# Kernel tuning notes

Hardware: AMD Instinct MI355X
Metric: run time of the kernel (lower is better)

Reference implementation:

```python
import jax
import jax.numpy as jnp
import numpy as np
from jax import lax

B, L, A, C = 32, 128, 64, 128  # batch, length, n_agents, channels (in == out)
KT = 3                          # temporal kernel size, padding (KT-1)//2 keeps length


def setup_inputs() -> dict:
    key = jax.random.key(0)
    k1, k2, k3 = jax.random.split(key, 3)
    x = jax.random.normal(k1, (B, L, A, C), dtype=jnp.float32)
    # Conv2d weight [out_ch, in_ch, kt, 1] and bias, kaiming-ish scale
    W = jax.random.normal(k2, (C, C, KT, 1), dtype=jnp.float32) * (1.0 / np.sqrt(C * KT))
    b = jax.random.normal(k3, (C,), dtype=jnp.float32) * 0.01
    return {"x": x, "W": W, "b": b}


def reference(x, W, b):
    # x: [B, L, A, C] -> [B, C, L, A] (torch NCHW layout with H=time, W=agents)
    length, n_agents = x.shape[1], x.shape[2]
    xc = jnp.transpose(x, (0, 3, 1, 2))
    res = xc  # residual is identity (input_dim == output_dim, t_stride == 1)
    pad_t = (KT - 1) // 2
    y = lax.conv_general_dilated(
        xc, W,
        window_strides=(1, 1),
        padding=[(pad_t, pad_t), (0, 0)],
        dimension_numbers=("NCHW", "OIHW", "NCHW"),
    ) + b[None, :, None, None]  # [B, C, L, A]
    # Dense graph g[t,a,t',a'] = 1 iff t==t' or a==a'.  einsum('ncv,vw->ncw', x, g)
    # is exactly: sum over same time (all agents) + sum over same agent (all times) - self.
    agent_sum = jnp.sum(y, axis=3, keepdims=True)  # [B, C, L, 1]
    time_sum = jnp.sum(y, axis=2, keepdims=True)   # [B, C, 1, A]
    scale = (length + n_agents - 2) ** 0.5
    g = (agent_sum + time_sum - y) / scale
    out = jax.nn.relu(g + res)
    return jnp.transpose(out, (0, 2, 3, 1))  # [B, L, A, C]
```

## Files before the change

### kernel.cpp

```cpp
#include <hip/hip_runtime.h>
#include <stdint.h>


typedef __attribute__((ext_vector_type(8))) short bf16x8;
typedef __attribute__((ext_vector_type(4))) float f32x4;

__device__ __forceinline__ uint32_t f2bf(float f) {
    union { float f; uint32_t u; } v; v.f = f;
    return (v.u + 0x7FFFu + ((v.u >> 16) & 1u)) >> 16;
}
__device__ __forceinline__ float bf2f(uint32_t h) {
    union { uint32_t u; float f; } v; v.u = h << 16; return v.f;
}
__device__ __forceinline__ uint32_t pk2(float lo, float hi) {
    return f2bf(lo) | (f2bf(hi) << 16);
}
__device__ __forceinline__ void gll16(const void* g, void* l) {
    __builtin_amdgcn_global_load_lds((const __attribute__((address_space(1))) void*)g,
                                     (__attribute__((address_space(3))) void*)l, 16, 0, 0);
}

__global__ __launch_bounds__(256) void prep_kernel(
    const float* __restrict__ x, uint16_t* __restrict__ x16, uint16_t* __restrict__ xa16,
    const float* __restrict__ W, uint16_t* __restrict__ wp)
{
    const int tid = threadIdx.x;
    const int bid = blockIdx.x;
    if (bid >= 4160) {
        int o = (bid - 4160) * 256 + tid;
        int i = o & 7, lane = (o >> 3) & 63, nt = (o >> 9) & 7, ks = (o >> 12) & 3, d = o >> 14;
        int ci = ks * 32 + (lane >> 4) * 8 + i;
        int co = nt * 16 + (lane & 15);
        wp[o] = (uint16_t)f2bf(W[(co * 128 + ci) * 3 + d]);
        return;
    }
    const int b = bid / 130, tp = bid - b * 130;
    uint16_t* xo = x16 + (size_t)bid * 8192;
    if (tp == 0 || tp == 129) {
        const uint4 z = make_uint4(0, 0, 0, 0);
        #pragma unroll
        for (int k = 0; k < 4; ++k) *(uint4*)(xo + tid * 32 + k * 8) = z;
        if (tid < 16) *(uint4*)(xa16 + (size_t)bid * 128 + tid * 8) = z;
        return;
    }
    const int t = tp - 1;
    const int ci4 = (tid & 31) * 4, ag = tid >> 5;
    const float* xr = x + (size_t)(b * 128 + t) * 8192;
    float4 part = make_float4(0.f, 0.f, 0.f, 0.f);
    #pragma unroll
    for (int r = 0; r < 8; ++r) {
        const int a = ag * 8 + r;
        const float4 v = *(const float4*)(xr + a * 128 + ci4);
        part.x += v.x; part.y += v.y; part.z += v.z; part.w += v.w;
        uint2 p; p.x = pk2(v.x, v.y); p.y = pk2(v.z, v.w);
        *(uint2*)(xo + a * 128 + ci4) = p;
    }
    __shared__ float red[8][128];
    *(float4*)&red[ag][ci4] = part;
    __syncthreads();
    if (tid < 128) {
        float s = 0.f;
        #pragma unroll
        for (int i = 0; i < 8; ++i) s += red[i][tid];
        xa16[(size_t)bid * 128 + tid] = (uint16_t)f2bf(s);
    }
}

__global__ __launch_bounds__(256) void xt_kernel(
    const uint16_t* __restrict__ x16, float* __restrict__ xt)
{
    const int tid = threadIdx.x, bid = blockIdx.x;
    const int a = bid & 63, b = bid >> 6;
    const int ci8 = (tid & 15) * 8, tg = tid >> 4;
    const uint16_t* base = x16 + ((size_t)(b * 130 + 1 + tg) * 64 + a) * 128 + ci8;
    float s[8];
    #pragma unroll
    for (int j = 0; j < 8; ++j) s[j] = 0.f;
    #pragma unroll
    for (int r = 0; r < 8; ++r) {
        const uint4 v = *(const uint4*)(base + (size_t)r * 16 * 8192);
        s[0] += bf2f(v.x & 0xFFFFu); s[1] += bf2f(v.x >> 16);
        s[2] += bf2f(v.y & 0xFFFFu); s[3] += bf2f(v.y >> 16);
        s[4] += bf2f(v.z & 0xFFFFu); s[5] += bf2f(v.z >> 16);
        s[6] += bf2f(v.w & 0xFFFFu); s[7] += bf2f(v.w >> 16);
    }
    __shared__ float red[16][128];
    *(float4*)&red[tg][ci8]     = make_float4(s[0], s[1], s[2], s[3]);
    *(float4*)&red[tg][ci8 + 4] = make_float4(s[4], s[5], s[6], s[7]);
    __syncthreads();
    if (tid < 128) {
        float v = 0.f;
        #pragma unroll
        for (int i = 0; i < 16; ++i) v += red[i][tid];
        xt[(size_t)bid * 128 + tid] = v;
    }
}

__global__ __launch_bounds__(256, 2) void sums_kernel(
    const uint16_t* __restrict__ xa16, const float* __restrict__ xt,
    const uint16_t* __restrict__ x16, const uint16_t* __restrict__ wp,
    const float* __restrict__ bias, float* __restrict__ asum, float* __restrict__ tsum)
{
    __shared__ __align__(16) uint16_t slab[130 * 128];
    const int tid = threadIdx.x;
    const int lane = tid & 63, wid = tid >> 6;
    const int wm = wid >> 1, wn = wid & 1;
    const int lr = lane & 15, lg = lane >> 4;
    f32x4 acc[4][4];
    #pragma unroll
    for (int mi = 0; mi < 4; ++mi)
        #pragma unroll
        for (int ni = 0; ni < 4; ++ni) acc[mi][ni] = (f32x4)0.f;

    if (blockIdx.x < 32) {
        const int b = blockIdx.x;
        #pragma unroll
        for (int it = 0; it < 9; ++it) {
            const int gg = it * 256 + tid;
            if (gg < 2080) {
                const int row = gg >> 4, sp = gg & 15;
                const int sl = sp ^ (row & 7);
                *(uint4*)(slab + gg * 8) =
                    *(const uint4*)(xa16 + (size_t)(b * 130 + row) * 128 + sl * 8);
            }
        }
        __syncthreads();
        #pragma unroll
        for (int g = 0; g < 4; ++g)
            #pragma unroll
            for (int d = 0; d < 3; ++d) {
                bf16x8 bq[4], af[4];
                #pragma unroll
                for (int ni = 0; ni < 4; ++ni)
                    bq[ni] = *(const bf16x8*)(wp + (size_t)((((d * 4 + g) * 8) + wn * 4 + ni) * 64 + lane) * 8);
                #pragma unroll
                for (int mi = 0; mi < 4; ++mi) {
                    const int row = wm * 64 + mi * 16 + lr + d;
                    af[mi] = *(const bf16x8*)(slab + row * 128 + ((g * 4 + lg) ^ (row & 7)) * 8);
                }
                #pragma unroll
                for (int mi = 0; mi < 4; ++mi)
                    #pragma unroll
                    for (int ni = 0; ni < 4; ++ni)
                        acc[mi][ni] = __builtin_amdgcn_mfma_f32_16x16x32_bf16(af[mi], bq[ni], acc[mi][ni], 0, 0, 0);
            }
        #pragma unroll
        for (int ni = 0; ni < 4; ++ni) {
            const int col = wn * 64 + ni * 16 + lr;
            const float bv = 64.f * bias[col];
            #pragma unroll
            for (int mi = 0; mi < 4; ++mi)
                #pragma unroll
                for (int j = 0; j < 4; ++j) {
                    const int t = wm * 64 + mi * 16 + lg * 4 + j;
                    asum[((size_t)b * 128 + t) * 128 + col] = acc[mi][ni][j] + bv;
                }
        }
        return;
    }

    const int bid = blockIdx.x - 32;
    const int r = tid >> 1, h = tid & 1;
    const int grow = bid * 128 + r, sb = grow >> 6, sa = grow & 63;
    #pragma unroll
    for (int d = 0; d < 3; ++d) {
        {
            const float* Sp = xt + (size_t)grow * 128 + h * 64;
            const uint16_t* Ep = x16 + ((size_t)(sb * 130 + (d == 0 ? 128 : 1)) * 64 + sa) * 128 + h * 64;
            #pragma unroll
            for (int k = 0; k < 8; ++k) {
                float4 f0 = *(const float4*)(Sp + k * 8);
                float4 f1 = *(const float4*)(Sp + k * 8 + 4);
                if (d != 1) {
                    const uint4 e = *(const uint4*)(Ep + k * 8);
                    f0.x -= bf2f(e.x & 0xFFFFu); f0.y -= bf2f(e.x >> 16);
                    f0.z -= bf2f(e.y & 0xFFFFu); f0.w -= bf2f(e.y >> 16);
                    f1.x -= bf2f(e.z & 0xFFFFu); f1.y -= bf2f(e.z >> 16);
                    f1.z -= bf2f(e.w & 0xFFFFu); f1.w -= bf2f(e.w >> 16);
                }
                uint4 o;
                o.x = pk2(f0.x, f0.y); o.y = pk2(f0.z, f0.w);
                o.z = pk2(f1.x, f1.y); o.w = pk2(f1.z, f1.w);
                const int sl = h * 8 + k;
                *(uint4*)(slab + r * 128 + (sl ^ (r & 7)) * 8) = o;
            }
        }
        __syncthreads();
        #pragma unroll
        for (int g = 0; g < 4; ++g) {
            bf16x8 bq[4], af[4];
            #pragma unroll
            for (int ni = 0; ni < 4; ++ni)
                bq[ni] = *(const bf16x8*)(wp + (size_t)((((d * 4 + g) * 8) + wn * 4 + ni) * 64 + lane) * 8);
            #pragma unroll
            for (int mi = 0; mi < 4; ++mi) {
                const int row = wm * 64 + mi * 16 + lr;
                af[mi] = *(const bf16x8*)(slab + row * 128 + ((g * 4 + lg) ^ (row & 7)) * 8);
            }
            #pragma unroll
            for (int mi = 0; mi < 4; ++mi)
                #pragma unroll
                for (int ni = 0; ni < 4; ++ni)
                    acc[mi][ni] = __builtin_amdgcn_mfma_f32_16x16x32_bf16(af[mi], bq[ni], acc[mi][ni], 0, 0, 0);
        }
        __syncthreads();
    }
    #pragma unroll
    for (int ni = 0; ni < 4; ++ni) {
        const int col = wn * 64 + ni * 16 + lr;
        const float bv = 128.f * bias[col];
        #pragma unroll
        for (int mi = 0; mi < 4; ++mi)
            #pragma unroll
            for (int j = 0; j < 4; ++j) {
                const int rg = bid * 128 + wm * 64 + mi * 16 + lg * 4 + j;
                tsum[(size_t)rg * 128 + col] = acc[mi][ni][j] + bv;
            }
    }
}

__global__ __launch_bounds__(512, 6) void conv_kernel(
    const uint16_t* __restrict__ x16, const uint16_t* __restrict__ wp,
    const float* __restrict__ bias, const float* __restrict__ asum,
    const float* __restrict__ tsum, float* __restrict__ out)
{
    __shared__ __align__(16) uint16_t slab[192 * 128];
    const int tid = threadIdx.x;
    const int raw = blockIdx.x;
    const int bid = (raw & 7) * 512 + (raw >> 3);
    const int b = bid >> 7, t = bid & 127;
    const int lane = tid & 63, wid = tid >> 6;
    const int lr = lane & 15, lg = lane >> 4;

    #pragma unroll
    for (int k = 0; k < 6; ++k) {
        const int row = wid * 24 + k * 4 + lg;
        const int sl = lr ^ (row & 7);
        const uint16_t* src = x16 +
            ((size_t)((b * 130 + t + (row >> 6)) * 64 + (row & 63))) * 128 + sl * 8;
        gll16(src, slab + wid * 3072 + k * 512);
    }
    __syncthreads();

    f32x4 acc[4];
    #pragma unroll
    for (int mi = 0; mi < 4; ++mi) acc[mi] = (f32x4)0.f;

    #pragma unroll
    for (int g = 0; g < 4; ++g)
        #pragma unroll
        for (int d = 0; d < 3; ++d) {
            bf16x8 bq, af[4];
            bq = *(const bf16x8*)(wp + (size_t)((((d * 4 + g) * 8) + wid) * 64 + lane) * 8);
            #pragma unroll
            for (int mi = 0; mi < 4; ++mi) {
                const int row = d * 64 + mi * 16 + lr;
                af[mi] = *(const bf16x8*)(slab + row * 128 + ((g * 4 + lg) ^ (row & 7)) * 8);
            }
            #pragma unroll
            for (int mi = 0; mi < 4; ++mi)
                acc[mi] = __builtin_amdgcn_mfma_f32_16x16x32_bf16(af[mi], bq, acc[mi], 0, 0, 0);
        }
    __syncthreads();

    {
        const int col = wid * 16 + lr;
        const float bv = bias[col];
        #pragma unroll
        for (int mi = 0; mi < 4; ++mi)
            #pragma unroll
            for (int j = 0; j < 4; ++j) {
                const int a = mi * 16 + lg * 4 + j;
                slab[a * 128 + (col ^ ((a & 7) << 3))] = (uint16_t)f2bf(acc[mi][j] + bv);
            }
    }
    __syncthreads();

    {
        const float inv = 0.07254762501100116f;
        const int cg = tid & 15, rb = tid >> 4;
        const float* ap = asum + ((size_t)(b * 128 + t)) * 128 + cg * 8;
        const float4 as0 = *(const float4*)ap, as1 = *(const float4*)(ap + 4);
        const float av[8] = {as0.x, as0.y, as0.z, as0.w, as1.x, as1.y, as1.z, as1.w};
        #pragma unroll
        for (int j = 0; j < 2; ++j) {
            const int a = j * 32 + rb;
            const uint4 yv = *(const uint4*)(slab + a * 128 + ((cg * 8) ^ ((a & 7) << 3)));
            const uint4 xv = *(const uint4*)(slab + (a + 64) * 128 + ((cg * 8) ^ ((a & 7) << 3)));
            const float* tp = tsum + ((size_t)(b * 64 + a)) * 128 + cg * 8;
            const float4 ts0 = *(const float4*)tp, ts1 = *(const float4*)(tp + 4);
            float yy[8], xx[8];
            yy[0] = bf2f(yv.x & 0xFFFFu); yy[1] = bf2f(yv.x >> 16);
            yy[2] = bf2f(yv.y & 0xFFFFu); yy[3] = bf2f(yv.y >> 16);
            yy[4] = bf2f(yv.z & 0xFFFFu); yy[5] = bf2f(yv.z >> 16);
            yy[6] = bf2f(yv.w & 0xFFFFu); yy[7] = bf2f(yv.w >> 16);
            xx[0] = bf2f(xv.x & 0xFFFFu); xx[1] = bf2f(xv.x >> 16);
            xx[2] = bf2f(xv.y & 0xFFFFu); xx[3] = bf2f(xv.y >> 16);
            xx[4] = bf2f(xv.z & 0xFFFFu); xx[5] = bf2f(xv.z >> 16);
            xx[6] = bf2f(xv.w & 0xFFFFu); xx[7] = bf2f(xv.w >> 16);
            const float tv[8] = {ts0.x, ts0.y, ts0.z, ts0.w, ts1.x, ts1.y, ts1.z, ts1.w};
            float o[8];
            #pragma unroll
            for (int i = 0; i < 8; ++i) {
                const float gg = (av[i] + tv[i] - yy[i]) * inv + xx[i];
                o[i] = gg > 0.f ? gg : 0.f;
            }
            float* op = out + ((size_t)((b * 128 + t) * 64 + a)) * 128 + cg * 8;
            *(float4*)op       = make_float4(o[0], o[1], o[2], o[3]);
            *(float4*)(op + 4) = make_float4(o[4], o[5], o[6], o[7]);
        }
    }
}

extern "C" void kernel_launch(void* const* d_in, const int* in_sizes, int n_in,
                              void* d_out, int out_size, void* d_ws, size_t ws_size,
                              hipStream_t stream) {
    const float* x    = (const float*)d_in[0];
    const float* W    = (const float*)d_in[1];
    const float* bias = (const float*)d_in[2];
    float* out = (float*)d_out;

    char* ws = (char*)d_ws;
    uint16_t* x16  = (uint16_t*)(ws);
    uint16_t* wp   = (uint16_t*)(ws + 68157440);
    uint16_t* xa16 = (uint16_t*)(ws + 68157440 + 98304);
    float* xt      = (float*)(ws + 68157440 + 98304 + 1064960);
    float* asum    = (float*)(ws + 68157440 + 98304 + 1064960 + 1048576);
    float* tsum    = (float*)(ws + 68157440 + 98304 + 1064960 + 1048576 + 2097152);

    prep_kernel <<<4352, 256, 0, stream>>>(x, x16, xa16, W, wp);
    xt_kernel   <<<2048, 256, 0, stream>>>(x16, xt);
    sums_kernel <<<48,   256, 0, stream>>>(xa16, xt, x16, wp, bias, asum, tsum);
    conv_kernel <<<4096, 512, 0, stream>>>(x16, wp, bias, asum, tsum, out);
}
```

Baseline: 117.7 us.

## Halve conv LDS slab by staging channels in two chunks; widen prep loads

```diff
diff --git a/kernel.cpp b/kernel.cpp
--- a/kernel.cpp
+++ b/kernel.cpp
@@ -44,25 +44,32 @@
         return;
     }
     const int t = tp - 1;
-    const int ci4 = (tid & 31) * 4, ag = tid >> 5;
+    const int ci8 = (tid & 15) * 8, ag = tid >> 4;
     const float* xr = x + (size_t)(b * 128 + t) * 8192;
-    float4 part = make_float4(0.f, 0.f, 0.f, 0.f);
-    #pragma unroll
-    for (int r = 0; r < 8; ++r) {
-        const int a = ag * 8 + r;
-        const float4 v = *(const float4*)(xr + a * 128 + ci4);
-        part.x += v.x; part.y += v.y; part.z += v.z; part.w += v.w;
-        uint2 p; p.x = pk2(v.x, v.y); p.y = pk2(v.z, v.w);
-        *(uint2*)(xo + a * 128 + ci4) = p;
-    }
-    __shared__ float red[8][128];
-    *(float4*)&red[ag][ci4] = part;
+    float s[8];
+    #pragma unroll
+    for (int j = 0; j < 8; ++j) s[j] = 0.f;
+    #pragma unroll
+    for (int r = 0; r < 4; ++r) {
+        const int a = ag * 4 + r;
+        const float4 v0 = *(const float4*)(xr + a * 128 + ci8);
+        const float4 v1 = *(const float4*)(xr + a * 128 + ci8 + 4);
+        s[0] += v0.x; s[1] += v0.y; s[2] += v0.z; s[3] += v0.w;
+        s[4] += v1.x; s[5] += v1.y; s[6] += v1.z; s[7] += v1.w;
+        uint4 p;
+        p.x = pk2(v0.x, v0.y); p.y = pk2(v0.z, v0.w);
+        p.z = pk2(v1.x, v1.y); p.w = pk2(v1.z, v1.w);
+        *(uint4*)(xo + a * 128 + ci8) = p;
+    }
+    __shared__ float red[16][128];
+    *(float4*)&red[ag][ci8]     = make_float4(s[0], s[1], s[2], s[3]);
+    *(float4*)&red[ag][ci8 + 4] = make_float4(s[4], s[5], s[6], s[7]);
     __syncthreads();
     if (tid < 128) {
-        float s = 0.f;
-        #pragma unroll
-        for (int i = 0; i < 8; ++i) s += red[i][tid];
-        xa16[(size_t)bid * 128 + tid] = (uint16_t)f2bf(s);
+        float v = 0.f;
+        #pragma unroll
+        for (int i = 0; i < 16; ++i) v += red[i][tid];
+        xa16[(size_t)bid * 128 + tid] = (uint16_t)f2bf(v);
     }
 }
 
@@ -219,12 +226,12 @@
     }
 }
 
-__global__ __launch_bounds__(512, 6) void conv_kernel(
+__global__ __launch_bounds__(512, 8) void conv_kernel(
     const uint16_t* __restrict__ x16, const uint16_t* __restrict__ wp,
     const float* __restrict__ bias, const float* __restrict__ asum,
     const float* __restrict__ tsum, float* __restrict__ out)
 {
-    __shared__ __align__(16) uint16_t slab[192 * 128];
+    __shared__ __align__(16) uint16_t slab[192 * 64];
     const int tid = threadIdx.x;
     const int raw = blockIdx.x;
     const int bid = (raw & 7) * 512 + (raw >> 3);
@@ -232,46 +239,65 @@
     const int lane = tid & 63, wid = tid >> 6;
     const int lr = lane & 15, lg = lane >> 4;
 
-    #pragma unroll
-    for (int k = 0; k < 6; ++k) {
-        const int row = wid * 24 + k * 4 + lg;
-        const int sl = lr ^ (row & 7);
-        const uint16_t* src = x16 +
-            ((size_t)((b * 130 + t + (row >> 6)) * 64 + (row & 63))) * 128 + sl * 8;
-        gll16(src, slab + wid * 3072 + k * 512);
-    }
-    __syncthreads();
-
     f32x4 acc[4];
     #pragma unroll
     for (int mi = 0; mi < 4; ++mi) acc[mi] = (f32x4)0.f;
 
-    #pragma unroll
-    for (int g = 0; g < 4; ++g)
-        #pragma unroll
-        for (int d = 0; d < 3; ++d) {
-            bf16x8 bq, af[4];
-            bq = *(const bf16x8*)(wp + (size_t)((((d * 4 + g) * 8) + wid) * 64 + lane) * 8);
-            #pragma unroll
-            for (int mi = 0; mi < 4; ++mi) {
-                const int row = d * 64 + mi * 16 + lr;
-                af[mi] = *(const bf16x8*)(slab + row * 128 + ((g * 4 + lg) ^ (row & 7)) * 8);
-            }
-            #pragma unroll
-            for (int mi = 0; mi < 4; ++mi)
-                acc[mi] = __builtin_amdgcn_mfma_f32_16x16x32_bf16(af[mi], bq, acc[mi], 0, 0, 0);
-        }
-    __syncthreads();
+#define STAGE(c) do {                                                          \
+    _Pragma("unroll")                                                          \
+    for (int k = 0; k < 3; ++k) {                                              \
+        const int row = wid * 24 + k * 8 + (lane >> 3);                        \
+        const int gran = (lane & 7) ^ (row & 7);                               \
+        const uint16_t* src = x16 +                                            \
+            ((size_t)((b * 130 + t + (row >> 6)) * 64 + (row & 63))) * 128 +   \
+            (c) * 64 + gran * 8;                                               \
+        gll16(src, slab + wid * 1536 + k * 512);                               \
+    } } while (0)
+
+#define MFMA_CHUNK(c) do {                                                     \
+    _Pragma("unroll")                                                          \
+    for (int d = 0; d < 3; ++d)                                                \
+        _Pragma("unroll")                                                      \
+        for (int g2 = 0; g2 < 2; ++g2) {                                       \
+            const int ks = (c) * 2 + g2;                                       \
+            bf16x8 bq, af[4];                                                  \
+            bq = *(const bf16x8*)(wp +                                         \
+                (size_t)((((d * 4 + ks) * 8) + wid) * 64 + lane) * 8);         \
+            _Pragma("unroll")                                                  \
+            for (int mi = 0; mi < 4; ++mi) {                                   \
+                const int row = d * 64 + mi * 16 + lr;                         \
+                af[mi] = *(const bf16x8*)(slab + row * 64 +                    \
+                    (((g2 * 4 + lg) ^ (row & 7)) * 8));                        \
+            }                                                                  \
+            _Pragma("unroll")                                                  \
+            for (int mi = 0; mi < 4; ++mi)                                     \
+                acc[mi] = __builtin_amdgcn_mfma_f32_16x16x32_bf16(             \
+                    af[mi], bq, acc[mi], 0, 0, 0);                             \
+        } } while (0)
+
+    STAGE(0);
+    __syncthreads();
+    MFMA_CHUNK(0);
+    __syncthreads();
+    STAGE(1);
+    __syncthreads();
+    MFMA_CHUNK(1);
+    __syncthreads();
+
+#undef STAGE
+#undef MFMA_CHUNK
 
     {
         const int col = wid * 16 + lr;
         const float bv = bias[col];
+        const int cl = col & 63;
+        const int rbase = (col >> 6) << 7;
         #pragma unroll
         for (int mi = 0; mi < 4; ++mi)
             #pragma unroll
             for (int j = 0; j < 4; ++j) {
                 const int a = mi * 16 + lg * 4 + j;
-                slab[a * 128 + (col ^ ((a & 7) << 3))] = (uint16_t)f2bf(acc[mi][j] + bv);
+                slab[(rbase + a) * 64 + (cl ^ ((a & 7) << 3))] = (uint16_t)f2bf(acc[mi][j] + bv);
             }
     }
     __syncthreads();
@@ -282,11 +308,19 @@
         const float* ap = asum + ((size_t)(b * 128 + t)) * 128 + cg * 8;
         const float4 as0 = *(const float4*)ap, as1 = *(const float4*)(ap + 4);
         const float av[8] = {as0.x, as0.y, as0.z, as0.w, as1.x, as1.y, as1.z, as1.w};
+        const int cl8 = (cg & 7) * 8;
         #pragma unroll
         for (int j = 0; j < 2; ++j) {
             const int a = j * 32 + rb;
-            const uint4 yv = *(const uint4*)(slab + a * 128 + ((cg * 8) ^ ((a & 7) << 3)));
-            const uint4 xv = *(const uint4*)(slab + (a + 64) * 128 + ((cg * 8) ^ ((a & 7) << 3)));
+            const int swz = cl8 ^ ((a & 7) << 3);
+            uint4 yv, xv;
+            if (cg < 8) {
+                yv = *(const uint4*)(slab + a * 64 + swz);
+                xv = *(const uint4*)(x16 + ((size_t)((b * 130 + t + 1) * 64 + a)) * 128 + cg * 8);
+            } else {
+                yv = *(const uint4*)(slab + (128 + a) * 64 + swz);
+                xv = *(const uint4*)(slab + (64 + a) * 64 + swz);
+            }
             const float* tp = tsum + ((size_t)(b * 64 + a)) * 128 + cg * 8;
             const float4 ts0 = *(const float4*)tp, ts1 = *(const float4*)(tp + 4);
             float yy[8], xx[8];
```

Measured after the change: 115.7 us. About the same (-1.7%).
